# Kernel tuning notes

Measured on AMD Instinct MI355X. Metric: run time of the kernel, lower is better.

Reference implementation:

```python
import jax, jax.numpy as jnp
import numpy as np

NSPINS = 2  # spin_split = 2 -> equal split into 2 spins


def setup_inputs() -> dict:
    key = jax.random.key(0)
    ks = jax.random.split(key, 6)
    B, N, D1, D2, ND = 4096, 32, 256, 32, 256
    scale1 = 1.0 / np.sqrt(D1)
    in_1e = jax.random.normal(ks[0], (B, N, D1), dtype=jnp.float32)
    in_2e = jax.random.normal(ks[1], (B, N, N, D2), dtype=jnp.float32)
    W_unmixed = jax.random.normal(ks[2], (D1, ND), dtype=jnp.float32) * scale1
    b_unmixed = jnp.zeros((ND,), dtype=jnp.float32)
    W_mixed = jax.random.normal(ks[3], (D1 * NSPINS, ND), dtype=jnp.float32) * (1.0 / np.sqrt(D1 * NSPINS))
    W_2e = jax.random.normal(ks[4], (D2 * NSPINS, ND), dtype=jnp.float32) * (1.0 / np.sqrt(D2 * NSPINS))
    return {"in_1e": in_1e, "in_2e": in_2e, "W_unmixed": W_unmixed,
            "b_unmixed": b_unmixed, "W_mixed": W_mixed, "W_2e": W_2e}


def _rolled_concat(arrays, n, axis=-1):
    return jnp.concatenate(arrays[n:] + arrays[:n], axis=axis)


def _ferminet_1e_layer(in_1e, in_2e, W_unmixed, b_unmixed, W_mixed, W_2e):
    # 1) unmixed: per-particle linear transform, (B, N, D1) -> (B, N, ND)
    dense_unmixed = in_1e @ W_unmixed + b_unmixed
    dense_unmixed_split = jnp.split(dense_unmixed, NSPINS, axis=-2)

    # 2) mixed: per-spin means, cyclic concat, shared linear (no bias)
    split_1e = jnp.split(in_1e, NSPINS, axis=-2)            # [i: (B, n_i, D1)]
    split_means = [jnp.mean(s, axis=-2, keepdims=True) for s in split_1e]  # [i: (B, 1, D1)]
    split_concat = [_rolled_concat(split_means, i) for i in range(NSPINS)]  # [i: (B, 1, D1*nspins)]
    all_spins_1e = jnp.concatenate(split_concat, axis=-2)   # (B, nspins, D1*nspins)
    dense_mixed = all_spins_1e @ W_mixed                    # (B, nspins, ND)
    dense_mixed_split = jnp.split(dense_mixed, NSPINS, axis=-2)  # [i: (B, 1, ND)]

    # 3) two-electron: spin-split on axis -3, mean over other-particle spin
    #    blocks on axis -2 (no keepdims), cyclic concat, shared linear (no bias)
    split_2e = jnp.split(in_2e, NSPINS, axis=-3)            # [i: (B, n_i, N, D2)]
    concat_2e = []
    for spin in range(NSPINS):
        sub = jnp.split(split_2e[spin], NSPINS, axis=-2)    # [j: (B, n_i, n_j, D2)]
        means = [jnp.mean(s, axis=-2) for s in sub]         # [j: (B, n_i, D2)]
        concat_2e.append(_rolled_concat(means, spin))       # (B, n_i, D2*nspins)
    all_spins_2e = jnp.concatenate(concat_2e, axis=-2)      # (B, N, D2*nspins)
    dense_2e = all_spins_2e @ W_2e                          # (B, N, ND)
    dense_2e_split = jnp.split(dense_2e, NSPINS, axis=-2)

    # combine per spin (mixed part broadcasts over the particle dim), activate
    out = jnp.concatenate(
        [dense_unmixed_split[i] + dense_mixed_split[i] + dense_2e_split[i]
         for i in range(NSPINS)], axis=-2)
    out = jnp.tanh(out)
    # residual skip connection (shapes match: D1 == ND)
    if in_1e.shape == out.shape:
        out = out + in_1e
    return out


def reference(in_1e, in_2e, W_unmixed, b_unmixed, W_mixed, W_2e):
    return _ferminet_1e_layer(in_1e, in_2e, W_unmixed, b_unmixed, W_mixed, W_2e)
```

## Files before the change

### kernel.cpp

```cpp
#include <hip/hip_runtime.h>
#include <math.h>


#define AS1 __attribute__((address_space(1)))
#define AS3 __attribute__((address_space(3)))

__device__ __forceinline__ void g2l16(const float* g, float* l) {
  __builtin_amdgcn_global_load_lds((const AS1 unsigned int*)g,
                                   (AS3 unsigned int*)l, 16, 0, 0);
}
__device__ __forceinline__ void g2l4(const float* g, float* l) {
  __builtin_amdgcn_global_load_lds((const AS1 unsigned int*)g,
                                   (AS3 unsigned int*)l, 4, 0, 0);
}

__device__ __forceinline__ float tanh_fast(float x) {
  float e = __expf(2.0f * x);
  return 1.0f - 2.0f / (e + 1.0f);
}

__global__ __launch_bounds__(256) void k_reduce2e(const float* __restrict__ in2e,
                                                  float* __restrict__ all2e) {
  const int t  = blockIdx.x * 256 + threadIdx.x;
  const int q  = t & 15;
  const int bi = t >> 4;
  const int i  = bi & 31;
  const int si = i >> 4;
  const int sj = (q < 8) ? si : 1 - si;
  const int d0 = (q & 7) << 2;
  const float4* src =
      reinterpret_cast<const float4*>(in2e + (size_t)bi * 1024 + sj * 512 + d0);
  float4 a = make_float4(0.f, 0.f, 0.f, 0.f);
#pragma unroll
  for (int p = 0; p < 16; ++p) {
    float4 v = src[p * 8];
    a.x += v.x; a.y += v.y; a.z += v.z; a.w += v.w;
  }
  const float s = 1.0f / 16.0f;
  reinterpret_cast<float4*>(all2e)[t] = make_float4(a.x*s, a.y*s, a.z*s, a.w*s);
}

__global__ __launch_bounds__(256, 2) void k_main(
    const float* __restrict__ in1e, const float* __restrict__ all2e,
    const float* __restrict__ Wu, const float* __restrict__ bu,
    const float* __restrict__ Wm, const float* __restrict__ W2e,
    float* __restrict__ out) {
  __shared__ float xs[32][260];
  __shared__ float ys[32][68];
  __shared__ float wbuf[32][256];
  __shared__ float m_lds[2][256];
  __shared__ float dm_lds[2][256];
  __shared__ float bias_lds[256];

  const int t = threadIdx.x;
  const int wave = t >> 6, lane = t & 63;
  const int b = blockIdx.x;

  {
    const float* x_src = in1e + (size_t)b * 8192;
#pragma unroll
    for (int rr = 0; rr < 8; ++rr) {
      int r = wave * 8 + rr;
      g2l16(x_src + r * 256 + lane * 4, &xs[r][0]);
    }
    const float* y_src = all2e + (size_t)b * 2048;
#pragma unroll
    for (int rr = 0; rr < 8; ++rr) {
      int r = wave * 8 + rr;
      g2l4(y_src + r * 64 + lane, &ys[r][0]);
    }
    if (wave == 0) g2l16(bu + lane * 4, &bias_lds[0]);
#pragma unroll
    for (int rr = 0; rr < 8; ++rr) {
      int r = wave * 8 + rr;
      g2l16(Wm + r * 256 + lane * 4, &wbuf[r][0]);
    }
  }
  __syncthreads();

  for (int idx = t; idx < 512; idx += 256) {
    const int sp = idx >> 8, k = idx & 255;
    float sum = 0.f;
#pragma unroll
    for (int ii = 0; ii < 16; ++ii) sum += xs[sp * 16 + ii][k];
    m_lds[sp][k] = sum * (1.0f / 16.0f);
  }
  __syncthreads();

  const int spm = t >> 7, c0m = (t & 127) * 2;
  const int i0 = (t >> 5) << 2, c0 = (t & 31) << 2;
  float dmx = 0.f, dmy = 0.f;
  float4 acc[4][2];
#pragma unroll
  for (int j = 0; j < 4; ++j) {
    acc[j][0] = make_float4(0.f, 0.f, 0.f, 0.f);
    acc[j][1] = make_float4(0.f, 0.f, 0.f, 0.f);
  }

  for (int c = 0; c < 26; ++c) {
    if (c < 16) {
      const float* mrow = (c < 8) ? &m_lds[spm][c * 32]
                                  : &m_lds[1 - spm][c * 32 - 256];
#pragma unroll
      for (int kk = 0; kk < 32; ++kk) {
        float a = mrow[kk];
        float2 w = *reinterpret_cast<const float2*>(&wbuf[kk][c0m]);
        dmx = fmaf(a, w.x, dmx);
        dmy = fmaf(a, w.y, dmy);
      }
      if (c == 15) { dm_lds[spm][c0m] = dmx; dm_lds[spm][c0m + 1] = dmy; }
    } else {
      const bool isX = (c < 24);
      const int kb = isX ? (c - 16) * 32 : (c - 24) * 32;
      const float* a0 = isX ? &xs[i0][kb] : &ys[i0][kb];
      const int as = isX ? 260 : 68;
#pragma unroll
      for (int k4 = 0; k4 < 8; ++k4) {
        float4 av[4], bA[4], bB[4];
#pragma unroll
        for (int j = 0; j < 4; ++j)
          av[j] = *reinterpret_cast<const float4*>(a0 + j * as + k4 * 4);
#pragma unroll
        for (int u = 0; u < 4; ++u) {
          bA[u] = *reinterpret_cast<const float4*>(&wbuf[k4 * 4 + u][c0]);
          bB[u] = *reinterpret_cast<const float4*>(&wbuf[k4 * 4 + u][c0 + 128]);
        }
#pragma unroll
        for (int u = 0; u < 4; ++u) {
#pragma unroll
          for (int j = 0; j < 4; ++j) {
            const float a = reinterpret_cast<const float*>(&av[j])[u];
            acc[j][0].x = fmaf(a, bA[u].x, acc[j][0].x);
            acc[j][0].y = fmaf(a, bA[u].y, acc[j][0].y);
            acc[j][0].z = fmaf(a, bA[u].z, acc[j][0].z);
            acc[j][0].w = fmaf(a, bA[u].w, acc[j][0].w);
            acc[j][1].x = fmaf(a, bB[u].x, acc[j][1].x);
            acc[j][1].y = fmaf(a, bB[u].y, acc[j][1].y);
            acc[j][1].z = fmaf(a, bB[u].z, acc[j][1].z);
            acc[j][1].w = fmaf(a, bB[u].w, acc[j][1].w);
          }
        }
      }
    }
    __syncthreads();
    if (c < 25) {
      const int cn = c + 1;
      const float* src = (cn < 16) ? (Wm + cn * 8192)
                       : (cn < 24) ? (Wu + (cn - 16) * 8192)
                                   : (W2e + (cn - 24) * 8192);
#pragma unroll
      for (int rr = 0; rr < 8; ++rr) {
        int r = wave * 8 + rr;
        g2l16(src + r * 256 + lane * 4, &wbuf[r][0]);
      }
      __syncthreads();
    }
  }

  const int sp = i0 >> 4;
  float4 bias0 = *reinterpret_cast<const float4*>(&bias_lds[c0]);
  float4 bias1 = *reinterpret_cast<const float4*>(&bias_lds[c0 + 128]);
  float4 dm0 = *reinterpret_cast<const float4*>(&dm_lds[sp][c0]);
  float4 dm1 = *reinterpret_cast<const float4*>(&dm_lds[sp][c0 + 128]);
  float4 cadd0 = make_float4(bias0.x + dm0.x, bias0.y + dm0.y,
                             bias0.z + dm0.z, bias0.w + dm0.w);
  float4 cadd1 = make_float4(bias1.x + dm1.x, bias1.y + dm1.y,
                             bias1.z + dm1.z, bias1.w + dm1.w);
#pragma unroll
  for (int j = 0; j < 4; ++j) {
    const int row = i0 + j;
    float* orow = out + (size_t)b * 8192 + row * 256;
    float4 r0 = *reinterpret_cast<const float4*>(&xs[row][c0]);
    float4 r1 = *reinterpret_cast<const float4*>(&xs[row][c0 + 128]);
    float4 v0, v1;
    v0.x = tanh_fast(acc[j][0].x + cadd0.x) + r0.x;
    v0.y = tanh_fast(acc[j][0].y + cadd0.y) + r0.y;
    v0.z = tanh_fast(acc[j][0].z + cadd0.z) + r0.z;
    v0.w = tanh_fast(acc[j][0].w + cadd0.w) + r0.w;
    v1.x = tanh_fast(acc[j][1].x + cadd1.x) + r1.x;
    v1.y = tanh_fast(acc[j][1].y + cadd1.y) + r1.y;
    v1.z = tanh_fast(acc[j][1].z + cadd1.z) + r1.z;
    v1.w = tanh_fast(acc[j][1].w + cadd1.w) + r1.w;
    *reinterpret_cast<float4*>(orow + c0) = v0;
    *reinterpret_cast<float4*>(orow + c0 + 128) = v1;
  }
}

extern "C" void kernel_launch(void* const* d_in, const int* in_sizes, int n_in,
                              void* d_out, int out_size, void* d_ws, size_t ws_size,
                              hipStream_t stream) {
  const float* in1e = (const float*)d_in[0];
  const float* in2e = (const float*)d_in[1];
  const float* Wu   = (const float*)d_in[2];
  const float* bu   = (const float*)d_in[3];
  const float* Wm   = (const float*)d_in[4];
  const float* W2e  = (const float*)d_in[5];
  float* out   = (float*)d_out;
  float* all2e = (float*)d_ws;

  hipLaunchKernelGGL(k_reduce2e, dim3(8192), dim3(256), 0, stream, in2e, all2e);
  hipLaunchKernelGGL(k_main, dim3(4096), dim3(256), 0, stream,
                     in1e, all2e, Wu, bu, Wm, W2e, out);
}
```

Measured before the change: 1.176 ms.

## Use split-bf16 MFMA for main GEMM and batch the mixed-mean projection

The fp32 FMA GEMM in the main kernel is replaced by bf16 MFMA 32x32x16 instructions, with a hi/lo split of both activations and weights (three products) to keep accuracy close to fp32. Weights are pre-packed into an MFMA-friendly bf16 layout in a small kernel. The mixed-spin projection moves into its own kernel that batches 8 samples per block, so each main block no longer streams the full Wm matrix. Per-sample means are computed alongside the 2e reduction. The change adds extra launches, workspace traffic and split conversion work, and its accuracy rests on the hi/lo bf16 decomposition.

```diff
diff --git a/kernel.cpp b/kernel.cpp
--- a/kernel.cpp
+++ b/kernel.cpp
@@ -5,13 +5,21 @@
 #define AS1 __attribute__((address_space(1)))
 #define AS3 __attribute__((address_space(3)))
 
-__device__ __forceinline__ void g2l16(const float* g, float* l) {
+typedef __attribute__((ext_vector_type(8))) short bf16x8;
+typedef __attribute__((ext_vector_type(16))) float f32x16;
+
+__device__ __forceinline__ void g2l16(const void* g, void* l) {
   __builtin_amdgcn_global_load_lds((const AS1 unsigned int*)g,
                                    (AS3 unsigned int*)l, 16, 0, 0);
 }
-__device__ __forceinline__ void g2l4(const float* g, float* l) {
-  __builtin_amdgcn_global_load_lds((const AS1 unsigned int*)g,
-                                   (AS3 unsigned int*)l, 4, 0, 0);
+
+__device__ __forceinline__ unsigned short f2bf(float f) {
+  unsigned u = __float_as_uint(f);
+  u += 0x7FFFu + ((u >> 16) & 1u);
+  return (unsigned short)(u >> 16);
+}
+__device__ __forceinline__ float bf2f(unsigned short h) {
+  return __uint_as_float(((unsigned)h) << 16);
 }
 
 __device__ __forceinline__ float tanh_fast(float x) {
@@ -19,170 +27,192 @@
   return 1.0f - 2.0f / (e + 1.0f);
 }
 
-__global__ __launch_bounds__(256) void k_reduce2e(const float* __restrict__ in2e,
-                                                  float* __restrict__ all2e) {
-  const int t  = blockIdx.x * 256 + threadIdx.x;
-  const int q  = t & 15;
-  const int bi = t >> 4;
-  const int i  = bi & 31;
-  const int si = i >> 4;
-  const int sj = (q < 8) ? si : 1 - si;
-  const int d0 = (q & 7) << 2;
-  const float4* src =
-      reinterpret_cast<const float4*>(in2e + (size_t)bi * 1024 + sj * 512 + d0);
-  float4 a = make_float4(0.f, 0.f, 0.f, 0.f);
-#pragma unroll
-  for (int p = 0; p < 16; ++p) {
-    float4 v = src[p * 8];
-    a.x += v.x; a.y += v.y; a.z += v.z; a.w += v.w;
-  }
-  const float s = 1.0f / 16.0f;
-  reinterpret_cast<float4*>(all2e)[t] = make_float4(a.x*s, a.y*s, a.z*s, a.w*s);
-}
-
-__global__ __launch_bounds__(256, 2) void k_main(
+#define OFF_ALL2E 0u
+#define OFF_MEANS 33554432u
+#define OFF_DM    41943040u
+#define OFF_WPK   50331648u
+
+__global__ __launch_bounds__(256) void k_A(const float* __restrict__ in1e,
+                                           const float* __restrict__ in2e,
+                                           float* __restrict__ all2e,
+                                           float* __restrict__ means) {
+  const int t = threadIdx.x, b = blockIdx.x;
+#pragma unroll
+  for (int rep = 0; rep < 2; ++rep) {
+    const int idx = rep * 256 + t;
+    const int q = idx & 15, i = idx >> 4;
+    const int si = i >> 4;
+    const int sj = (q < 8) ? si : 1 - si;
+    const float4* src = reinterpret_cast<const float4*>(in2e) +
+                        ((size_t)b * 8192 + i * 256 + sj * 128 + (q & 7));
+    float4 a = make_float4(0.f, 0.f, 0.f, 0.f);
+#pragma unroll
+    for (int p = 0; p < 16; ++p) {
+      float4 v = src[p * 8];
+      a.x += v.x; a.y += v.y; a.z += v.z; a.w += v.w;
+    }
+    const float s = 1.0f / 16.0f;
+    reinterpret_cast<float4*>(all2e)[(size_t)b * 512 + i * 16 + q] =
+        make_float4(a.x * s, a.y * s, a.z * s, a.w * s);
+  }
+#pragma unroll
+  for (int rep = 0; rep < 2; ++rep) {
+    const int idx = rep * 256 + t;
+    const int s = idx >> 8, k = idx & 255;
+    const float* base = in1e + (size_t)b * 8192 + (s * 16) * 256 + k;
+    float sum = 0.f;
+#pragma unroll
+    for (int ii = 0; ii < 16; ++ii) sum += base[ii * 256];
+    means[(size_t)b * 512 + s * 256 + k] = sum * (1.0f / 16.0f);
+  }
+}
+
+__global__ __launch_bounds__(256) void k_P(const float* __restrict__ Wu,
+                                           const float* __restrict__ W2e,
+                                           unsigned short* __restrict__ wpk) {
+  const int g = blockIdx.x * 256 + threadIdx.x;
+  const int l = g & 63, n = (g >> 6) & 7, v = (g >> 9) & 1, s = g >> 10;
+  const int c = n * 32 + (l & 31);
+  const int k0 = s * 16 + (l >> 5) * 8;
+  unsigned short h[8];
+#pragma unroll
+  for (int e = 0; e < 8; ++e) {
+    const int k = k0 + e;
+    const float w = (k < 256) ? Wu[k * 256 + c] : W2e[(k - 256) * 256 + c];
+    const unsigned short hi = f2bf(w);
+    h[e] = v ? f2bf(w - bf2f(hi)) : hi;
+  }
+  *reinterpret_cast<uint4*>(wpk + (size_t)g * 8) = *reinterpret_cast<uint4*>(h);
+}
+
+__global__ __launch_bounds__(256) void k_B(const float* __restrict__ means,
+                                           const float* __restrict__ Wm,
+                                           float* __restrict__ dm) {
+  __shared__ float cm[16][512];
+  const int t = threadIdx.x;
+  const int b0 = blockIdx.x * 8;
+#pragma unroll
+  for (int j = 0; j < 32; ++j) {
+    const int idx = t + 256 * j;
+    const int r = idx >> 9, k = idx & 511;
+    const int s = r & 1, bb = r >> 1, b = b0 + bb;
+    const float mval = (k < 256) ? means[(size_t)b * 512 + s * 256 + k]
+                                 : means[(size_t)b * 512 + (1 - s) * 256 + (k - 256)];
+    cm[r][k] = mval;
+  }
+  __syncthreads();
+  const int nd = t;
+  float acc[16];
+#pragma unroll
+  for (int r = 0; r < 16; ++r) acc[r] = 0.f;
+#pragma unroll 4
+  for (int k = 0; k < 512; ++k) {
+    const float w = Wm[(size_t)k * 256 + nd];
+#pragma unroll
+    for (int r = 0; r < 16; ++r) acc[r] = fmaf(cm[r][k], w, acc[r]);
+  }
+#pragma unroll
+  for (int r = 0; r < 16; ++r) {
+    const int s = r & 1, bb = r >> 1;
+    dm[(size_t)(b0 + bb) * 512 + s * 256 + nd] = acc[r];
+  }
+}
+
+__global__ __launch_bounds__(256, 2) void k_C(
     const float* __restrict__ in1e, const float* __restrict__ all2e,
-    const float* __restrict__ Wu, const float* __restrict__ bu,
-    const float* __restrict__ Wm, const float* __restrict__ W2e,
-    float* __restrict__ out) {
-  __shared__ float xs[32][260];
-  __shared__ float ys[32][68];
-  __shared__ float wbuf[32][256];
-  __shared__ float m_lds[2][256];
-  __shared__ float dm_lds[2][256];
-  __shared__ float bias_lds[256];
+    const float* __restrict__ bu, const float* __restrict__ dm,
+    const unsigned short* __restrict__ wpk, float* __restrict__ out) {
+  __shared__ unsigned short xh[20][64][8];
+  __shared__ unsigned short xl[20][64][8];
+  __shared__ unsigned short wbuf[2][8192];
+  __shared__ float dmb[2][256];
+  __shared__ float biasb[256];
 
   const int t = threadIdx.x;
-  const int wave = t >> 6, lane = t & 63;
+  const int w = t >> 6, lane = t & 63;
   const int b = blockIdx.x;
 
-  {
-    const float* x_src = in1e + (size_t)b * 8192;
-#pragma unroll
-    for (int rr = 0; rr < 8; ++rr) {
-      int r = wave * 8 + rr;
-      g2l16(x_src + r * 256 + lane * 4, &xs[r][0]);
+#pragma unroll
+  for (int jj = 0; jj < 4; ++jj) {
+    const int cb = (jj * 4 + w) * 64;
+    g2l16((const char*)wpk + (size_t)(cb + lane) * 16, &wbuf[0][cb * 8]);
+  }
+  if (w == 0) {
+    g2l16((const char*)(dm + (size_t)b * 512) + lane * 16, &dmb[0][0]);
+  } else if (w == 1) {
+    g2l16((const char*)(dm + (size_t)b * 512) + 1024 + lane * 16, &dmb[0][256]);
+  } else if (w == 2) {
+    g2l16((const char*)bu + lane * 16, &biasb[0]);
+  }
+
+#pragma unroll
+  for (int jj = 0; jj < 5; ++jj) {
+    const int chunk = t + 256 * jj;
+    const int s = chunk >> 6, l = chunk & 63;
+    const int row = l & 31, kh = l >> 5;
+    const float* gsrc;
+    if (s < 16) gsrc = in1e + (size_t)b * 8192 + row * 256 + s * 16 + kh * 8;
+    else        gsrc = all2e + (size_t)b * 2048 + row * 64 + (s - 16) * 16 + kh * 8;
+    const float4 v0 = *reinterpret_cast<const float4*>(gsrc);
+    const float4 v1 = *reinterpret_cast<const float4*>(gsrc + 4);
+    float f[8] = {v0.x, v0.y, v0.z, v0.w, v1.x, v1.y, v1.z, v1.w};
+    unsigned short hh[8], ll[8];
+#pragma unroll
+    for (int e = 0; e < 8; ++e) {
+      hh[e] = f2bf(f[e]);
+      ll[e] = f2bf(f[e] - bf2f(hh[e]));
     }
-    const float* y_src = all2e + (size_t)b * 2048;
-#pragma unroll
-    for (int rr = 0; rr < 8; ++rr) {
-      int r = wave * 8 + rr;
-      g2l4(y_src + r * 64 + lane, &ys[r][0]);
-    }
-    if (wave == 0) g2l16(bu + lane * 4, &bias_lds[0]);
-#pragma unroll
-    for (int rr = 0; rr < 8; ++rr) {
-      int r = wave * 8 + rr;
-      g2l16(Wm + r * 256 + lane * 4, &wbuf[r][0]);
-    }
+    *reinterpret_cast<uint4*>(&xh[s][l][0]) = *reinterpret_cast<uint4*>(hh);
+    *reinterpret_cast<uint4*>(&xl[s][l][0]) = *reinterpret_cast<uint4*>(ll);
   }
   __syncthreads();
 
-  for (int idx = t; idx < 512; idx += 256) {
-    const int sp = idx >> 8, k = idx & 255;
-    float sum = 0.f;
-#pragma unroll
-    for (int ii = 0; ii < 16; ++ii) sum += xs[sp * 16 + ii][k];
-    m_lds[sp][k] = sum * (1.0f / 16.0f);
-  }
-  __syncthreads();
-
-  const int spm = t >> 7, c0m = (t & 127) * 2;
-  const int i0 = (t >> 5) << 2, c0 = (t & 31) << 2;
-  float dmx = 0.f, dmy = 0.f;
-  float4 acc[4][2];
-#pragma unroll
-  for (int j = 0; j < 4; ++j) {
-    acc[j][0] = make_float4(0.f, 0.f, 0.f, 0.f);
-    acc[j][1] = make_float4(0.f, 0.f, 0.f, 0.f);
-  }
-
-  for (int c = 0; c < 26; ++c) {
-    if (c < 16) {
-      const float* mrow = (c < 8) ? &m_lds[spm][c * 32]
-                                  : &m_lds[1 - spm][c * 32 - 256];
-#pragma unroll
-      for (int kk = 0; kk < 32; ++kk) {
-        float a = mrow[kk];
-        float2 w = *reinterpret_cast<const float2*>(&wbuf[kk][c0m]);
-        dmx = fmaf(a, w.x, dmx);
-        dmy = fmaf(a, w.y, dmy);
-      }
-      if (c == 15) { dm_lds[spm][c0m] = dmx; dm_lds[spm][c0m + 1] = dmy; }
-    } else {
-      const bool isX = (c < 24);
-      const int kb = isX ? (c - 16) * 32 : (c - 24) * 32;
-      const float* a0 = isX ? &xs[i0][kb] : &ys[i0][kb];
-      const int as = isX ? 260 : 68;
-#pragma unroll
-      for (int k4 = 0; k4 < 8; ++k4) {
-        float4 av[4], bA[4], bB[4];
-#pragma unroll
-        for (int j = 0; j < 4; ++j)
-          av[j] = *reinterpret_cast<const float4*>(a0 + j * as + k4 * 4);
-#pragma unroll
-        for (int u = 0; u < 4; ++u) {
-          bA[u] = *reinterpret_cast<const float4*>(&wbuf[k4 * 4 + u][c0]);
-          bB[u] = *reinterpret_cast<const float4*>(&wbuf[k4 * 4 + u][c0 + 128]);
-        }
-#pragma unroll
-        for (int u = 0; u < 4; ++u) {
-#pragma unroll
-          for (int j = 0; j < 4; ++j) {
-            const float a = reinterpret_cast<const float*>(&av[j])[u];
-            acc[j][0].x = fmaf(a, bA[u].x, acc[j][0].x);
-            acc[j][0].y = fmaf(a, bA[u].y, acc[j][0].y);
-            acc[j][0].z = fmaf(a, bA[u].z, acc[j][0].z);
-            acc[j][0].w = fmaf(a, bA[u].w, acc[j][0].w);
-            acc[j][1].x = fmaf(a, bB[u].x, acc[j][1].x);
-            acc[j][1].y = fmaf(a, bB[u].y, acc[j][1].y);
-            acc[j][1].z = fmaf(a, bB[u].z, acc[j][1].z);
-            acc[j][1].w = fmaf(a, bB[u].w, acc[j][1].w);
-          }
-        }
+  f32x16 acc0 = {}, acc1 = {};
+  const int n0 = w * 2, n1 = w * 2 + 1;
+  for (int s = 0; s < 20; ++s) {
+    const int cur = s & 1;
+    if (s < 19) {
+      const unsigned short* src = wpk + (size_t)(s + 1) * 8192;
+#pragma unroll
+      for (int jj = 0; jj < 4; ++jj) {
+        const int cb = (jj * 4 + w) * 64;
+        g2l16((const char*)src + (size_t)(cb + lane) * 16,
+              &wbuf[cur ^ 1][cb * 8]);
       }
     }
+    const bf16x8 ah = *reinterpret_cast<const bf16x8*>(&xh[s][lane][0]);
+    const bf16x8 al = *reinterpret_cast<const bf16x8*>(&xl[s][lane][0]);
+    const bf16x8 bh0 = *reinterpret_cast<const bf16x8*>(
+        &wbuf[cur][((0 * 8 + n0) * 64 + lane) * 8]);
+    const bf16x8 bh1 = *reinterpret_cast<const bf16x8*>(
+        &wbuf[cur][((0 * 8 + n1) * 64 + lane) * 8]);
+    const bf16x8 bl0 = *reinterpret_cast<const bf16x8*>(
+        &wbuf[cur][((1 * 8 + n0) * 64 + lane) * 8]);
+    const bf16x8 bl1 = *reinterpret_cast<const bf16x8*>(
+        &wbuf[cur][((1 * 8 + n1) * 64 + lane) * 8]);
+    acc0 = __builtin_amdgcn_mfma_f32_32x32x16_bf16(ah, bh0, acc0, 0, 0, 0);
+    acc1 = __builtin_amdgcn_mfma_f32_32x32x16_bf16(ah, bh1, acc1, 0, 0, 0);
+    acc0 = __builtin_amdgcn_mfma_f32_32x32x16_bf16(ah, bl0, acc0, 0, 0, 0);
+    acc1 = __builtin_amdgcn_mfma_f32_32x32x16_bf16(ah, bl1, acc1, 0, 0, 0);
+    acc0 = __builtin_amdgcn_mfma_f32_32x32x16_bf16(al, bh0, acc0, 0, 0, 0);
+    acc1 = __builtin_amdgcn_mfma_f32_32x32x16_bf16(al, bh1, acc1, 0, 0, 0);
     __syncthreads();
-    if (c < 25) {
-      const int cn = c + 1;
-      const float* src = (cn < 16) ? (Wm + cn * 8192)
-                       : (cn < 24) ? (Wu + (cn - 16) * 8192)
-                                   : (W2e + (cn - 24) * 8192);
-#pragma unroll
-      for (int rr = 0; rr < 8; ++rr) {
-        int r = wave * 8 + rr;
-        g2l16(src + r * 256 + lane * 4, &wbuf[r][0]);
-      }
-      __syncthreads();
-    }
-  }
-
-  const int sp = i0 >> 4;
-  float4 bias0 = *reinterpret_cast<const float4*>(&bias_lds[c0]);
-  float4 bias1 = *reinterpret_cast<const float4*>(&bias_lds[c0 + 128]);
-  float4 dm0 = *reinterpret_cast<const float4*>(&dm_lds[sp][c0]);
-  float4 dm1 = *reinterpret_cast<const float4*>(&dm_lds[sp][c0 + 128]);
-  float4 cadd0 = make_float4(bias0.x + dm0.x, bias0.y + dm0.y,
-                             bias0.z + dm0.z, bias0.w + dm0.w);
-  float4 cadd1 = make_float4(bias1.x + dm1.x, bias1.y + dm1.y,
-                             bias1.z + dm1.z, bias1.w + dm1.w);
-#pragma unroll
-  for (int j = 0; j < 4; ++j) {
-    const int row = i0 + j;
-    float* orow = out + (size_t)b * 8192 + row * 256;
-    float4 r0 = *reinterpret_cast<const float4*>(&xs[row][c0]);
-    float4 r1 = *reinterpret_cast<const float4*>(&xs[row][c0 + 128]);
-    float4 v0, v1;
-    v0.x = tanh_fast(acc[j][0].x + cadd0.x) + r0.x;
-    v0.y = tanh_fast(acc[j][0].y + cadd0.y) + r0.y;
-    v0.z = tanh_fast(acc[j][0].z + cadd0.z) + r0.z;
-    v0.w = tanh_fast(acc[j][0].w + cadd0.w) + r0.w;
-    v1.x = tanh_fast(acc[j][1].x + cadd1.x) + r1.x;
-    v1.y = tanh_fast(acc[j][1].y + cadd1.y) + r1.y;
-    v1.z = tanh_fast(acc[j][1].z + cadd1.z) + r1.z;
-    v1.w = tanh_fast(acc[j][1].w + cadd1.w) + r1.w;
-    *reinterpret_cast<float4*>(orow + c0) = v0;
-    *reinterpret_cast<float4*>(orow + c0 + 128) = v1;
+  }
+
+  const int colA = n0 * 32 + (lane & 31);
+  const int colB = n1 * 32 + (lane & 31);
+  const float ca = biasb[colA], cb_ = biasb[colB];
+#pragma unroll
+  for (int r = 0; r < 16; ++r) {
+    const int row = (r & 3) + 8 * (r >> 2) + 4 * (lane >> 5);
+    const int sp = row >> 4;
+    const size_t base = (size_t)b * 8192 + row * 256;
+    float vA = acc0[r] + ca + dmb[sp][colA];
+    float vB = acc1[r] + cb_ + dmb[sp][colB];
+    vA = tanh_fast(vA) + in1e[base + colA];
+    vB = tanh_fast(vB) + in1e[base + colB];
+    out[base + colA] = vA;
+    out[base + colB] = vB;
   }
 }
 
@@ -195,10 +225,16 @@
   const float* bu   = (const float*)d_in[3];
   const float* Wm   = (const float*)d_in[4];
   const float* W2e  = (const float*)d_in[5];
-  float* out   = (float*)d_out;
-  float* all2e = (float*)d_ws;
-
-  hipLaunchKernelGGL(k_reduce2e, dim3(8192), dim3(256), 0, stream, in2e, all2e);
-  hipLaunchKernelGGL(k_main, dim3(4096), dim3(256), 0, stream,
-                     in1e, all2e, Wu, bu, Wm, W2e, out);
-}
+  float* out = (float*)d_out;
+
+  char* ws = (char*)d_ws;
+  float* all2e = (float*)(ws + OFF_ALL2E);
+  float* means = (float*)(ws + OFF_MEANS);
+  float* dm    = (float*)(ws + OFF_DM);
+  unsigned short* wpk = (unsigned short*)(ws + OFF_WPK);
+
+  hipLaunchKernelGGL(k_A, dim3(4096), dim3(256), 0, stream, in1e, in2e, all2e, means);
+  hipLaunchKernelGGL(k_P, dim3(80),   dim3(256), 0, stream, Wu, W2e, wpk);
+  hipLaunchKernelGGL(k_B, dim3(512),  dim3(256), 0, stream, means, Wm, dm);
+  hipLaunchKernelGGL(k_C, dim3(4096), dim3(256), 0, stream, in1e, all2e, bu, dm, wpk, out);
+}
```

After: 1.005 ms. -14.6%, faster.
